# Optimization experiments

Hardware: AMD Instinct MI355X
Metric: run time of the kernel (lower is better)

## Reference

```python
import jax, jax.numpy as jnp
import numpy as np

N_NODES = 100000
N_EDGES = 3200000
N_GRAPHS = 256
DIMS = [38, 64, 32, 16]


def setup_inputs() -> dict:
    key = jax.random.key(0)
    ks = jax.random.split(key, 16)
    x = jax.random.normal(ks[0], (N_NODES, DIMS[0]), dtype=jnp.float32)
    edge_index = jax.random.randint(ks[1], (2, N_EDGES), 0, N_NODES, dtype=jnp.int64)
    batch_vec = jnp.sort(jax.random.randint(ks[2], (N_NODES,), 0, N_GRAPHS, dtype=jnp.int64))
    inp = {"x": x, "edge_index": edge_index, "batch_vec": batch_vec}
    # Per layer l: W_rel [out,in] (with bias b [out]), W_root [out,in] (no bias)
    ki = 3
    for l in range(3):
        din, dout = DIMS[l], DIMS[l + 1]
        s = 1.0 / np.sqrt(din)
        inp[f"W_rel{l}"] = jax.random.uniform(ks[ki], (dout, din), minval=-s, maxval=s, dtype=jnp.float32); ki += 1
        inp[f"b{l}"] = jax.random.uniform(ks[ki], (dout,), minval=-s, maxval=s, dtype=jnp.float32); ki += 1
        inp[f"W_root{l}"] = jax.random.uniform(ks[ki], (dout, din), minval=-s, maxval=s, dtype=jnp.float32); ki += 1
    return inp


def _graph_conv(x, src, dst, W_rel, b, W_root):
    # sum_{j -> i} x_j, then linear (equivalent to summing transformed messages)
    agg = jax.ops.segment_sum(x[src], dst, num_segments=N_NODES)  # [N, din]
    return agg @ W_rel.T + b + x @ W_root.T


def reference(x, edge_index, batch_vec, W_rel0, b0, W_root0, W_rel1, b1, W_root1, W_rel2, b2, W_root2):
    src, dst = edge_index[0], edge_index[1]
    h = jnp.tanh(_graph_conv(x, src, dst, W_rel0, b0, W_root0))
    h = jnp.tanh(_graph_conv(h, src, dst, W_rel1, b1, W_root1))
    h = _graph_conv(h, src, dst, W_rel2, b2, W_root2)
    # global mean pool over graphs
    sums = jax.ops.segment_sum(h, batch_vec, num_segments=N_GRAPHS)  # [G, 16]
    counts = jax.ops.segment_sum(jnp.ones((N_NODES,), dtype=h.dtype), batch_vec, num_segments=N_GRAPHS)
    pooled = sums / jnp.maximum(counts, 1.0)[:, None]
    return jnp.tanh(pooled)
```

## Files before the change

kernel.cpp:

```cpp
#include <hip/hip_runtime.h>
#include <math.h>

#define N_NODES  100000
#define N_EDGES  3200000
#define N_GRAPHS 256


#define BSHIFT 8
#define NB ((N_NODES + 255) >> 8)
#define NBLK 1280
#define EPB ((N_EDGES + NBLK - 1) / NBLK)

typedef _Float16 f16;
typedef _Float16 f16x2 __attribute__((ext_vector_type(2)));

__device__ __forceinline__ float fast_tanh(float x) {
    x = fminf(20.f, fmaxf(-20.f, x));
    float e = __expf(2.f * x);
    return (e - 1.f) / (e + 1.f);
}

__device__ __forceinline__ unsigned int pack_bf2(float a, float b) {
    unsigned int ua = __float_as_uint(a);
    unsigned int ub = __float_as_uint(b);
    ua += 0x7fffu + ((ua >> 16) & 1u);
    ub += 0x7fffu + ((ub >> 16) & 1u);
    return (ua >> 16) | (ub & 0xffff0000u);
}

__device__ __forceinline__ f16x2 u2h(unsigned int u) { union { unsigned int u; f16x2 h; } c; c.u = u; return c.h; }
__device__ __forceinline__ unsigned int h2u(f16x2 h) { union { unsigned int u; f16x2 h; } c; c.h = h; return c.u; }
__device__ __forceinline__ unsigned int mkh2(float a, float b) {
    f16x2 v; v.x = (f16)a; v.y = (f16)b; return h2u(v);
}

__device__ __forceinline__ float fdot2f(f16x2 a, f16x2 b, float c) {
#if __has_builtin(__builtin_amdgcn_fdot2)
    return __builtin_amdgcn_fdot2(a, b, c, false);
#else
    return c + (float)a.x * (float)b.x + (float)a.y * (float)b.y;
#endif
}


__global__ __launch_bounds__(256) void k_hist(const int* __restrict__ dst,
                                              int* __restrict__ bucket_cnt,
                                              int* __restrict__ blockoff) {
    __shared__ int hist[NB];
    int tid = threadIdx.x;
    int b = blockIdx.x;
    for (int i = tid; i < NB; i += 256) hist[i] = 0;
    __syncthreads();
    int lo = b * EPB;
    int hi = min(lo + EPB, N_EDGES);
    for (int e = lo + tid; e < hi; e += 256)
        atomicAdd(&hist[dst[e] >> BSHIFT], 1);
    __syncthreads();
    for (int i = tid; i < NB; i += 256) {
        int c = hist[i];
        blockoff[b * NB + i] = (c > 0) ? atomicAdd(&bucket_cnt[i], c) : 0;
    }
}

__global__ __launch_bounds__(512) void k_scan_buckets(const int* __restrict__ bucket_cnt,
                                                      int* __restrict__ bucket_base) {
    __shared__ int sd[512];
    int tid = threadIdx.x;
    int v = (tid < NB) ? bucket_cnt[tid] : 0;
    int val = v;
    sd[tid] = val;
    __syncthreads();
#pragma unroll
    for (int off = 1; off < 512; off <<= 1) {
        int t = (tid >= off) ? sd[tid - off] : 0;
        __syncthreads();
        val += t;
        sd[tid] = val;
        __syncthreads();
    }
    if (tid < NB) {
        bucket_base[tid] = val - v;
        if (tid == NB - 1) bucket_base[NB] = val;
    }
}

__global__ __launch_bounds__(256) void k_scatter_buckets(const int* __restrict__ src,
                                                         const int* __restrict__ dst,
                                                         const int* __restrict__ bucket_base,
                                                         const int* __restrict__ blockoff,
                                                         int* __restrict__ ebuf) {
    __shared__ int base[NB];
    __shared__ int cur[NB];
    int tid = threadIdx.x;
    int b = blockIdx.x;
    for (int i = tid; i < NB; i += 256) {
        base[i] = bucket_base[i] + blockoff[b * NB + i];
        cur[i] = 0;
    }
    __syncthreads();
    int lo = b * EPB;
    int hi = min(lo + EPB, N_EDGES);
    for (int e = lo + tid; e < hi; e += 256) {
        int d = dst[e];
        int bin = d >> BSHIFT;
        int r = atomicAdd(&cur[bin], 1);
        ebuf[base[bin] + r] = src[e] | ((d & 255) << 17);
    }
}

__global__ __launch_bounds__(256) void k_bucket_csr(const int* __restrict__ ebuf,
                                                    const int* __restrict__ bucket_base,
                                                    int* __restrict__ rowptr,
                                                    int* __restrict__ rowend,
                                                    int* __restrict__ elist) {
    __shared__ int cnt[256];
    __shared__ int nb[256];
    __shared__ int cur[256];
    __shared__ int sscan[256];
    int b = blockIdx.x;
    int tid = threadIdx.x;
    int e0 = bucket_base[b];
    int e1 = bucket_base[b + 1];
    cnt[tid] = 0;
    cur[tid] = 0;
    __syncthreads();
    for (int j = e0 + tid; j < e1; j += 256)
        atomicAdd(&cnt[ebuf[j] >> 17], 1);
    __syncthreads();
    int v = cnt[tid];
    int val = v;
    sscan[tid] = val;
    __syncthreads();
#pragma unroll
    for (int off = 1; off < 256; off <<= 1) {
        int t = (tid >= off) ? sscan[tid - off] : 0;
        __syncthreads();
        val += t;
        sscan[tid] = val;
        __syncthreads();
    }
    int excl = val - v;
    nb[tid] = excl;
    int node = (b << BSHIFT) + tid;
    if (node < N_NODES) {
        rowptr[node] = e0 + excl;
        rowend[node] = e0 + val;
    }
    __syncthreads();
    for (int j = e0 + tid; j < e1; j += 256) {
        int w = ebuf[j];
        int dl = w >> 17;
        int r = atomicAdd(&cur[dl], 1);
        elist[e0 + nb[dl] + r] = w & 0x1FFFF;
    }
}

__global__ __launch_bounds__(256) void k_cast_bf16(const float* __restrict__ in,
                                                   unsigned int* __restrict__ out,
                                                   int n_pairs) {
    int i = blockIdx.x * 256 + threadIdx.x;
    if (i >= n_pairs) return;
    float2 v = ((const float2*)in)[i];
    out[i] = pack_bf2(v.x, v.y);
}

template<int DIM2>
__global__ __launch_bounds__(256) void k_gather_bf16(const unsigned int* __restrict__ feat,
                                                     const int* __restrict__ rowptr,
                                                     const int* __restrict__ rowend,
                                                     const int* __restrict__ elist,
                                                     float* __restrict__ agg) {
    int idx = blockIdx.x * 256 + threadIdx.x;
    if (idx >= N_NODES * DIM2) return;
    int n = idx / DIM2;
    int p = idx - n * DIM2;
    int j = rowptr[n];
    int e = rowend[n];
    float a0 = 0.f, a1 = 0.f;
    for (; j + 3 < e; j += 4) {
        int s0 = elist[j];
        int s1 = elist[j + 1];
        int s2 = elist[j + 2];
        int s3 = elist[j + 3];
        unsigned int w0 = feat[s0 * DIM2 + p];
        unsigned int w1 = feat[s1 * DIM2 + p];
        unsigned int w2 = feat[s2 * DIM2 + p];
        unsigned int w3 = feat[s3 * DIM2 + p];
        a0 += __uint_as_float(w0 << 16);
        a1 += __uint_as_float(w0 & 0xffff0000u);
        a0 += __uint_as_float(w1 << 16);
        a1 += __uint_as_float(w1 & 0xffff0000u);
        a0 += __uint_as_float(w2 << 16);
        a1 += __uint_as_float(w2 & 0xffff0000u);
        a0 += __uint_as_float(w3 << 16);
        a1 += __uint_as_float(w3 & 0xffff0000u);
    }
    for (; j < e; ++j) {
        unsigned int w = feat[elist[j] * DIM2 + p];
        a0 += __uint_as_float(w << 16);
        a1 += __uint_as_float(w & 0xffff0000u);
    }
    agg[n * (2 * DIM2) + 2 * p]     = a0;
    agg[n * (2 * DIM2) + 2 * p + 1] = a1;
}

__global__ __launch_bounds__(256) void k_fused0(const float* __restrict__ agg,
                                                const float* __restrict__ x,
                                                const float* __restrict__ Wrel0,
                                                const float* __restrict__ b0,
                                                const float* __restrict__ Wroot0,
                                                const float* __restrict__ Wrel1,
                                                const float* __restrict__ b1,
                                                const float* __restrict__ Wroot1,
                                                unsigned int* __restrict__ y1b,
                                                float* __restrict__ r1) {
    __shared__ unsigned int sWr[64 * 20];
    __shared__ unsigned int sWt[64 * 20];
    __shared__ unsigned int sW1r[32 * 32];
    __shared__ unsigned int sW1t[32 * 32];
    __shared__ float sb0[64];
    __shared__ float sb1[32];
    int tid = threadIdx.x;
    for (int i = tid; i < 64 * 20; i += 256) {
        int o = i / 20, d = i - o * 20;
        float a0 = (2 * d     < 38) ? Wrel0[o * 38 + 2 * d]     : 0.f;
        float a1 = (2 * d + 1 < 38) ? Wrel0[o * 38 + 2 * d + 1] : 0.f;
        float t0 = (2 * d     < 38) ? Wroot0[o * 38 + 2 * d]     : 0.f;
        float t1 = (2 * d + 1 < 38) ? Wroot0[o * 38 + 2 * d + 1] : 0.f;
        sWr[i] = mkh2(a0, a1);
        sWt[i] = mkh2(t0, t1);
    }
    for (int i = tid; i < 32 * 32; i += 256) {
        int op = i >> 5, j = i & 31;
        sW1r[i] = mkh2(Wrel1[j * 64 + 2 * op], Wrel1[j * 64 + 2 * op + 1]);
        sW1t[i] = mkh2(Wroot1[j * 64 + 2 * op], Wroot1[j * 64 + 2 * op + 1]);
    }
    if (tid < 64) sb0[tid] = b0[tid];
    if (tid < 32) sb1[tid] = b1[tid];
    __syncthreads();

    int lane = tid & 63;
    int ph = lane & 31;
    int sh = lane >> 5;
    int n0 = blockIdx.x * 256 + (tid >> 6) * 64 + 2 * ph;
    if (n0 >= N_NODES) return;
    int n1 = n0 + 1;

    unsigned int xa0[20], xx0[20], xa1[20], xx1[20];
    {
        const float2* A0 = (const float2*)(agg + (size_t)n0 * 38);
        const float2* X0 = (const float2*)(x   + (size_t)n0 * 38);
        const float2* A1 = (const float2*)(agg + (size_t)n1 * 38);
        const float2* X1 = (const float2*)(x   + (size_t)n1 * 38);
#pragma unroll
        for (int i = 0; i < 19; ++i) {
            float2 v;
            v = A0[i]; xa0[i] = mkh2(v.x, v.y);
            v = X0[i]; xx0[i] = mkh2(v.x, v.y);
            v = A1[i]; xa1[i] = mkh2(v.x, v.y);
            v = X1[i]; xx1[i] = mkh2(v.x, v.y);
        }
        xa0[19] = 0; xx0[19] = 0; xa1[19] = 0; xx1[19] = 0;
    }

    unsigned int hp0[16], hp1[16];
    int obase = sh * 32;
#pragma unroll
    for (int i = 0; i < 16; ++i) {
        float h00 = 0.f, h01 = 0.f, h10 = 0.f, h11 = 0.f;
#pragma unroll
        for (int par = 0; par < 2; ++par) {
            int o = obase + 2 * i + par;
            float c0 = sb0[o], c1 = 0.f, c2 = 0.f, c3 = 0.f;
            float d0 = sb0[o], d1 = 0.f, d2 = 0.f, d3 = 0.f;
            const uint4* wr = (const uint4*)(sWr + o * 20);
            const uint4* wt = (const uint4*)(sWt + o * 20);
#pragma unroll
            for (int q = 0; q < 5; ++q) {
                uint4 w = wr[q];
                c0 = fdot2f(u2h(xa0[4 * q + 0]), u2h(w.x), c0);
                c1 = fdot2f(u2h(xa0[4 * q + 1]), u2h(w.y), c1);
                c2 = fdot2f(u2h(xa0[4 * q + 2]), u2h(w.z), c2);
                c3 = fdot2f(u2h(xa0[4 * q + 3]), u2h(w.w), c3);
                d0 = fdot2f(u2h(xa1[4 * q + 0]), u2h(w.x), d0);
                d1 = fdot2f(u2h(xa1[4 * q + 1]), u2h(w.y), d1);
                d2 = fdot2f(u2h(xa1[4 * q + 2]), u2h(w.z), d2);
                d3 = fdot2f(u2h(xa1[4 * q + 3]), u2h(w.w), d3);
                uint4 v = wt[q];
                c0 = fdot2f(u2h(xx0[4 * q + 0]), u2h(v.x), c0);
                c1 = fdot2f(u2h(xx0[4 * q + 1]), u2h(v.y), c1);
                c2 = fdot2f(u2h(xx0[4 * q + 2]), u2h(v.z), c2);
                c3 = fdot2f(u2h(xx0[4 * q + 3]), u2h(v.w), c3);
                d0 = fdot2f(u2h(xx1[4 * q + 0]), u2h(v.x), d0);
                d1 = fdot2f(u2h(xx1[4 * q + 1]), u2h(v.y), d1);
                d2 = fdot2f(u2h(xx1[4 * q + 2]), u2h(v.z), d2);
                d3 = fdot2f(u2h(xx1[4 * q + 3]), u2h(v.w), d3);
            }
            float hA = fast_tanh(c0 + c1 + c2 + c3);
            float hB = fast_tanh(d0 + d1 + d2 + d3);
            if (par == 0) { h00 = hA; h10 = hB; }
            else          { h01 = hA; h11 = hB; }
        }
        hp0[i] = mkh2(h00, h01);
        hp1[i] = mkh2(h10, h11);
    }

    unsigned int H0[32], H1[32];
#pragma unroll
    for (int i = 0; i < 16; ++i) {
        unsigned int g0 = (unsigned int)__shfl_xor((int)hp0[i], 32);
        unsigned int g1 = (unsigned int)__shfl_xor((int)hp1[i], 32);
        if (sh == 0) { H0[i] = hp0[i]; H0[16 + i] = g0; H1[i] = hp1[i]; H1[16 + i] = g1; }
        else         { H0[i] = g0; H0[16 + i] = hp0[i]; H1[i] = g1; H1[16 + i] = hp1[i]; }
    }

    int jb = sh * 16;
    float y0[16], r0[16], y1v[16], r1v[16];
#pragma unroll
    for (int j = 0; j < 16; ++j) {
        y0[j] = 0.f; y1v[j] = 0.f;
        float bb = sb1[jb + j];
        r0[j] = bb; r1v[j] = bb;
    }
#pragma unroll
    for (int op = 0; op < 32; ++op) {
        f16x2 h0 = u2h(H0[op]);
        f16x2 h1 = u2h(H1[op]);
        const uint4* w1 = (const uint4*)(sW1r + op * 32 + jb);
        const uint4* w2 = (const uint4*)(sW1t + op * 32 + jb);
#pragma unroll
        for (int q = 0; q < 4; ++q) {
            uint4 a = w1[q], b = w2[q];
            y0[4 * q + 0] = fdot2f(h0, u2h(a.x), y0[4 * q + 0]);
            y0[4 * q + 1] = fdot2f(h0, u2h(a.y), y0[4 * q + 1]);
            y0[4 * q + 2] = fdot2f(h0, u2h(a.z), y0[4 * q + 2]);
            y0[4 * q + 3] = fdot2f(h0, u2h(a.w), y0[4 * q + 3]);
            y1v[4 * q + 0] = fdot2f(h1, u2h(a.x), y1v[4 * q + 0]);
            y1v[4 * q + 1] = fdot2f(h1, u2h(a.y), y1v[4 * q + 1]);
            y1v[4 * q + 2] = fdot2f(h1, u2h(a.z), y1v[4 * q + 2]);
            y1v[4 * q + 3] = fdot2f(h1, u2h(a.w), y1v[4 * q + 3]);
            r0[4 * q + 0] = fdot2f(h0, u2h(b.x), r0[4 * q + 0]);
            r0[4 * q + 1] = fdot2f(h0, u2h(b.y), r0[4 * q + 1]);
            r0[4 * q + 2] = fdot2f(h0, u2h(b.z), r0[4 * q + 2]);
            r0[4 * q + 3] = fdot2f(h0, u2h(b.w), r0[4 * q + 3]);
            r1v[4 * q + 0] = fdot2f(h1, u2h(b.x), r1v[4 * q + 0]);
            r1v[4 * q + 1] = fdot2f(h1, u2h(b.y), r1v[4 * q + 1]);
            r1v[4 * q + 2] = fdot2f(h1, u2h(b.z), r1v[4 * q + 2]);
            r1v[4 * q + 3] = fdot2f(h1, u2h(b.w), r1v[4 * q + 3]);
        }
    }

    unsigned int* yo0 = y1b + (size_t)n0 * 16 + (jb >> 1);
    unsigned int* yo1 = y1b + (size_t)n1 * 16 + (jb >> 1);
#pragma unroll
    for (int p = 0; p < 8; ++p) {
        yo0[p] = pack_bf2(y0[2 * p], y0[2 * p + 1]);
        yo1[p] = pack_bf2(y1v[2 * p], y1v[2 * p + 1]);
    }
    float4* ro0 = (float4*)(r1 + (size_t)n0 * 32 + jb);
    float4* ro1 = (float4*)(r1 + (size_t)n1 * 32 + jb);
#pragma unroll
    for (int q = 0; q < 4; ++q) {
        ro0[q] = make_float4(r0[4 * q], r0[4 * q + 1], r0[4 * q + 2], r0[4 * q + 3]);
        ro1[q] = make_float4(r1v[4 * q], r1v[4 * q + 1], r1v[4 * q + 2], r1v[4 * q + 3]);
    }
}

__global__ __launch_bounds__(256) void k_fused1(const float* __restrict__ agg,
                                                const float* __restrict__ r1,
                                                const float* __restrict__ Wrel2,
                                                float* __restrict__ h2,
                                                unsigned int* __restrict__ y2b)
{
    __shared__ float sW[32 * 16];
    int tid = threadIdx.x;
    for (int i = tid; i < 512; i += 256) {
        int k = i >> 4, j = i & 15;
        sW[i] = Wrel2[j * 32 + k];
    }
    __syncthreads();
    int n = blockIdx.x * 256 + tid;
    if (n >= N_NODES) return;
    const float4* a4 = (const float4*)(agg + (size_t)n * 32);
    const float4* r4 = (const float4*)(r1 + (size_t)n * 32);
    float h[32];
#pragma unroll
    for (int i = 0; i < 8; ++i) {
        float4 a = a4[i], r = r4[i];
        h[4 * i]     = fast_tanh(a.x + r.x);
        h[4 * i + 1] = fast_tanh(a.y + r.y);
        h[4 * i + 2] = fast_tanh(a.z + r.z);
        h[4 * i + 3] = fast_tanh(a.w + r.w);
    }
    float4* ho = (float4*)(h2 + (size_t)n * 32);
#pragma unroll
    for (int i = 0; i < 8; ++i) ho[i] = make_float4(h[4 * i], h[4 * i + 1], h[4 * i + 2], h[4 * i + 3]);
    float y[16];
#pragma unroll
    for (int j = 0; j < 16; ++j) y[j] = 0.f;
#pragma unroll
    for (int k = 0; k < 32; ++k) {
        const float4* w = (const float4*)(sW + k * 16);
#pragma unroll
        for (int j = 0; j < 4; ++j) {
            float4 wv = w[j];
            y[4 * j]     += h[k] * wv.x; y[4 * j + 1] += h[k] * wv.y;
            y[4 * j + 2] += h[k] * wv.z; y[4 * j + 3] += h[k] * wv.w;
        }
    }
    unsigned int* yo = y2b + (size_t)n * 8;
#pragma unroll
    for (int p = 0; p < 8; ++p) yo[p] = pack_bf2(y[2 * p], y[2 * p + 1]);
}

__global__ __launch_bounds__(256) void k_graph_start(const int* __restrict__ batch,
                                                     int* __restrict__ gstart) {
    int i = blockIdx.x * 256 + threadIdx.x;
    if (i >= N_NODES) return;
    int g = batch[i];
    int gp = (i == 0) ? -1 : batch[i - 1];
    for (int gg = gp + 1; gg <= g; ++gg) gstart[gg] = i;
    if (i == N_NODES - 1)
        for (int gg = g + 1; gg <= N_GRAPHS; ++gg) gstart[gg] = N_NODES;
}

__global__ __launch_bounds__(256) void k_pool(const float* __restrict__ agg,
                                              const float* __restrict__ h2,
                                              const int* __restrict__ gstart,
                                              float* __restrict__ psum)
{
    __shared__ float part[4][48];
    int g = blockIdx.x;
    int wave = threadIdx.x >> 6;
    int lane = threadIdx.x & 63;
    int s = gstart[g], e = gstart[g + 1];
    if (lane < 48) {
        float a0 = 0.f, a1 = 0.f;
        if (lane < 16) {
            int n = s + wave;
            for (; n + 4 < e; n += 8) {
                a0 += agg[n * 16 + lane];
                a1 += agg[(n + 4) * 16 + lane];
            }
            if (n < e) a0 += agg[n * 16 + lane];
        } else {
            int d = lane - 16;
            int n = s + wave;
            for (; n + 4 < e; n += 8) {
                a0 += h2[n * 32 + d];
                a1 += h2[(n + 4) * 32 + d];
            }
            if (n < e) a0 += h2[n * 32 + d];
        }
        part[wave][lane] = a0 + a1;
    }
    __syncthreads();
    if (threadIdx.x < 48)
        psum[g * 48 + threadIdx.x] = part[0][threadIdx.x] + part[1][threadIdx.x]
                                   + part[2][threadIdx.x] + part[3][threadIdx.x];
}

__global__ __launch_bounds__(256) void k_finalize2(const float* __restrict__ psum,
                                                   const float* __restrict__ Wroot,
                                                   const float* __restrict__ b,
                                                   const int* __restrict__ gstart,
                                                   float* __restrict__ out) {
    __shared__ float sW[16 * 32];
    __shared__ float sb[16];
    int tid = threadIdx.x;
    for (int i = tid; i < 16 * 32; i += 256) sW[i] = Wroot[i];
    if (tid < 16) sb[tid] = b[tid];
    __syncthreads();
    int idx = blockIdx.x * 256 + tid;
    if (idx >= N_GRAPHS * 16) return;
    int g = idx >> 4;
    int o = idx & 15;
    float cnt = (float)(gstart[g + 1] - gstart[g]);
    const float* p = psum + g * 48;
    float acc = p[o] + cnt * sb[o];
#pragma unroll
    for (int k = 0; k < 32; ++k) acc += p[16 + k] * sW[o * 32 + k];
    out[idx] = fast_tanh(acc / fmaxf(cnt, 1.f));
}

extern "C" void kernel_launch(void* const* d_in, const int* in_sizes, int n_in,
                              void* d_out, int out_size, void* d_ws, size_t ws_size,
                              hipStream_t stream) {
    const float* x      = (const float*)d_in[0];
    const int*   eidx   = (const int*)d_in[1];
    const int*   src    = eidx;
    const int*   dst    = eidx + N_EDGES;
    const int*   batch  = (const int*)d_in[2];
    const float* Wrel0  = (const float*)d_in[3];
    const float* b0     = (const float*)d_in[4];
    const float* Wroot0 = (const float*)d_in[5];
    const float* Wrel1  = (const float*)d_in[6];
    const float* b1     = (const float*)d_in[7];
    const float* Wroot1 = (const float*)d_in[8];
    const float* Wrel2  = (const float*)d_in[9];
    const float* b2     = (const float*)d_in[10];
    const float* Wroot2 = (const float*)d_in[11];
    float* out = (float*)d_out;

    float* ws   = (float*)d_ws;
    float* agg  = ws;
    float* r1   = agg + (size_t)N_NODES * 38;
    float* h2   = r1  + (size_t)N_NODES * 32;
    unsigned int* ybuf = (unsigned int*)(h2 + (size_t)N_NODES * 32);
    float* psum = (float*)(ybuf + (size_t)N_NODES * 16);
    int* rowptr      = (int*)(psum + N_GRAPHS * 48);
    int* rowend      = rowptr + N_NODES;
    int* gstart      = rowend + N_NODES;
    int* bucket_cnt  = gstart + 260;
    int* bucket_base = bucket_cnt + 400;
    int* blockoff    = bucket_base + 400;
    int* elist       = blockoff + (size_t)NBLK * NB;
    int* ebuf        = (int*)h2;
    unsigned int* xb = (unsigned int*)r1;

    k_cast_bf16<<<(N_NODES * 19 + 255) / 256, 256, 0, stream>>>(x, xb, N_NODES * 19);

    hipMemsetAsync(bucket_cnt, 0, sizeof(int) * NB, stream);
    k_hist<<<NBLK, 256, 0, stream>>>(dst, bucket_cnt, blockoff);
    k_scan_buckets<<<1, 512, 0, stream>>>(bucket_cnt, bucket_base);
    k_scatter_buckets<<<NBLK, 256, 0, stream>>>(src, dst, bucket_base, blockoff, ebuf);
    k_bucket_csr<<<NB, 256, 0, stream>>>(ebuf, bucket_base, rowptr, rowend, elist);
    k_graph_start<<<(N_NODES + 255) / 256, 256, 0, stream>>>(batch, gstart);

    k_gather_bf16<19><<<(N_NODES * 19 + 255) / 256, 256, 0, stream>>>(xb, rowptr, rowend, elist, agg);
    k_fused0<<<(N_NODES + 255) / 256, 256, 0, stream>>>(agg, x, Wrel0, b0, Wroot0,
                                                        Wrel1, b1, Wroot1, ybuf, r1);

    k_gather_bf16<16><<<(N_NODES * 16 + 255) / 256, 256, 0, stream>>>(ybuf, rowptr, rowend, elist, agg);
    k_fused1<<<(N_NODES + 255) / 256, 256, 0, stream>>>(agg, r1, Wrel2, h2, ybuf);

    k_gather_bf16<8><<<(N_NODES * 8 + 255) / 256, 256, 0, stream>>>(ybuf, rowptr, rowend, elist, agg);

    k_pool<<<N_GRAPHS, 256, 0, stream>>>(agg, h2, gstart, psum);
    k_finalize2<<<(N_GRAPHS * 16 + 255) / 256, 256, 0, stream>>>(psum, Wroot2, b2, gstart, out);
}
```

Baseline: 353.1 us.

## Split bf16 feature tables into column slices for cache-resident gathers

Stores the bf16 node features as separate column-slice arrays (8/8/3 words for the input, 8/8 for layer 1) and gathers each slice in its own pass, writing into the strided fp32 aggregate buffer. Each slice table is smaller (3.2 MB per 8-word slice), so the random-neighbour gathers are more likely to hit in L2/MALL and waste fewer cache lines. In exchange the edge list and row pointers are read once per slice and there are more kernel launches. It also halves the number of histogram/scatter blocks used to build the CSR.

```diff
diff --git a/kernel.cpp b/kernel.cpp
--- a/kernel.cpp
+++ b/kernel.cpp
@@ -8,7 +8,7 @@
 
 #define BSHIFT 8
 #define NB ((N_NODES + 255) >> 8)
-#define NBLK 1280
+#define NBLK 640
 #define EPB ((N_EDGES + NBLK - 1) / NBLK)
 
 typedef _Float16 f16;
@@ -155,21 +155,27 @@
     }
 }
 
-__global__ __launch_bounds__(256) void k_cast_bf16(const float* __restrict__ in,
-                                                   unsigned int* __restrict__ out,
-                                                   int n_pairs) {
+__global__ __launch_bounds__(256) void k_cast_slices(const float* __restrict__ in,
+                                                     unsigned int* __restrict__ s0,
+                                                     unsigned int* __restrict__ s1,
+                                                     unsigned int* __restrict__ s2) {
     int i = blockIdx.x * 256 + threadIdx.x;
-    if (i >= n_pairs) return;
+    if (i >= N_NODES * 19) return;
+    int n = i / 19;
+    int p = i - n * 19;
     float2 v = ((const float2*)in)[i];
-    out[i] = pack_bf2(v.x, v.y);
-}
-
-template<int DIM2>
-__global__ __launch_bounds__(256) void k_gather_bf16(const unsigned int* __restrict__ feat,
-                                                     const int* __restrict__ rowptr,
-                                                     const int* __restrict__ rowend,
-                                                     const int* __restrict__ elist,
-                                                     float* __restrict__ agg) {
+    unsigned int w = pack_bf2(v.x, v.y);
+    if (p < 8)       s0[n * 8 + p] = w;
+    else if (p < 16) s1[n * 8 + p - 8] = w;
+    else             s2[n * 3 + p - 16] = w;
+}
+
+template<int DIM2, int ASTRIDE, int OFF>
+__global__ __launch_bounds__(256) void k_gather_slice(const unsigned int* __restrict__ feat,
+                                                      const int* __restrict__ rowptr,
+                                                      const int* __restrict__ rowend,
+                                                      const int* __restrict__ elist,
+                                                      float* __restrict__ agg) {
     int idx = blockIdx.x * 256 + threadIdx.x;
     if (idx >= N_NODES * DIM2) return;
     int n = idx / DIM2;
@@ -200,8 +206,8 @@
         a0 += __uint_as_float(w << 16);
         a1 += __uint_as_float(w & 0xffff0000u);
     }
-    agg[n * (2 * DIM2) + 2 * p]     = a0;
-    agg[n * (2 * DIM2) + 2 * p + 1] = a1;
+    agg[n * ASTRIDE + OFF + 2 * p]     = a0;
+    agg[n * ASTRIDE + OFF + 2 * p + 1] = a1;
 }
 
 __global__ __launch_bounds__(256) void k_fused0(const float* __restrict__ agg,
@@ -212,7 +218,8 @@
                                                 const float* __restrict__ Wrel1,
                                                 const float* __restrict__ b1,
                                                 const float* __restrict__ Wroot1,
-                                                unsigned int* __restrict__ y1b,
+                                                unsigned int* __restrict__ y1b0,
+                                                unsigned int* __restrict__ y1b1,
                                                 float* __restrict__ r1) {
     __shared__ unsigned int sWr[64 * 20];
     __shared__ unsigned int sWt[64 * 20];
@@ -350,8 +357,8 @@
         }
     }
 
-    unsigned int* yo0 = y1b + (size_t)n0 * 16 + (jb >> 1);
-    unsigned int* yo1 = y1b + (size_t)n1 * 16 + (jb >> 1);
+    unsigned int* yo0 = (sh ? y1b1 : y1b0) + (size_t)n0 * 8;
+    unsigned int* yo1 = (sh ? y1b1 : y1b0) + (size_t)n1 * 8;
 #pragma unroll
     for (int p = 0; p < 8; ++p) {
         yo0[p] = pack_bf2(y0[2 * p], y0[2 * p + 1]);
@@ -516,9 +523,14 @@
     int* blockoff    = bucket_base + 400;
     int* elist       = blockoff + (size_t)NBLK * NB;
     int* ebuf        = (int*)h2;
-    unsigned int* xb = (unsigned int*)r1;
-
-    k_cast_bf16<<<(N_NODES * 19 + 255) / 256, 256, 0, stream>>>(x, xb, N_NODES * 19);
+    unsigned int* xb0 = (unsigned int*)r1;
+    unsigned int* xb1 = xb0 + (size_t)N_NODES * 8;
+    unsigned int* xb2 = xb1 + (size_t)N_NODES * 8;
+    unsigned int* y1b0 = ybuf;
+    unsigned int* y1b1 = ybuf + (size_t)N_NODES * 8;
+    unsigned int* y2b  = ybuf;
+
+    k_cast_slices<<<(N_NODES * 19 + 255) / 256, 256, 0, stream>>>(x, xb0, xb1, xb2);
 
     hipMemsetAsync(bucket_cnt, 0, sizeof(int) * NB, stream);
     k_hist<<<NBLK, 256, 0, stream>>>(dst, bucket_cnt, blockoff);
@@ -527,14 +539,17 @@
     k_bucket_csr<<<NB, 256, 0, stream>>>(ebuf, bucket_base, rowptr, rowend, elist);
     k_graph_start<<<(N_NODES + 255) / 256, 256, 0, stream>>>(batch, gstart);
 
-    k_gather_bf16<19><<<(N_NODES * 19 + 255) / 256, 256, 0, stream>>>(xb, rowptr, rowend, elist, agg);
+    k_gather_slice<8, 38, 0 ><<<(N_NODES * 8 + 255) / 256, 256, 0, stream>>>(xb0, rowptr, rowend, elist, agg);
+    k_gather_slice<8, 38, 16><<<(N_NODES * 8 + 255) / 256, 256, 0, stream>>>(xb1, rowptr, rowend, elist, agg);
+    k_gather_slice<3, 38, 32><<<(N_NODES * 3 + 255) / 256, 256, 0, stream>>>(xb2, rowptr, rowend, elist, agg);
     k_fused0<<<(N_NODES + 255) / 256, 256, 0, stream>>>(agg, x, Wrel0, b0, Wroot0,
-                                                        Wrel1, b1, Wroot1, ybuf, r1);
-
-    k_gather_bf16<16><<<(N_NODES * 16 + 255) / 256, 256, 0, stream>>>(ybuf, rowptr, rowend, elist, agg);
-    k_fused1<<<(N_NODES + 255) / 256, 256, 0, stream>>>(agg, r1, Wrel2, h2, ybuf);
-
-    k_gather_bf16<8><<<(N_NODES * 8 + 255) / 256, 256, 0, stream>>>(ybuf, rowptr, rowend, elist, agg);
+                                                        Wrel1, b1, Wroot1, y1b0, y1b1, r1);
+
+    k_gather_slice<8, 32, 0 ><<<(N_NODES * 8 + 255) / 256, 256, 0, stream>>>(y1b0, rowptr, rowend, elist, agg);
+    k_gather_slice<8, 32, 16><<<(N_NODES * 8 + 255) / 256, 256, 0, stream>>>(y1b1, rowptr, rowend, elist, agg);
+    k_fused1<<<(N_NODES + 255) / 256, 256, 0, stream>>>(agg, r1, Wrel2, h2, y2b);
+
+    k_gather_slice<8, 16, 0 ><<<(N_NODES * 8 + 255) / 256, 256, 0, stream>>>(y2b, rowptr, rowend, elist, agg);
 
     k_pool<<<N_GRAPHS, 256, 0, stream>>>(agg, h2, gstart, psum);
     k_finalize2<<<(N_GRAPHS * 16 + 255) / 256, 256, 0, stream>>>(psum, Wroot2, b2, gstart, out);
```

Result: no change. 352.9 us (-0.0%).
